# Kernel optimization log

Hardware: AMD Instinct MI355X
Metric: run time of the kernel (lower is better)

Reference implementation:

```python
import jax, jax.numpy as jnp
import numpy as np

PATCH = 8
EPS = 1e-5


def setup_inputs() -> dict:
    key = jax.random.key(0)
    k0, k1, k2 = jax.random.split(key, 3)
    B, C, H, W = 8, 256, 256, 256
    r = 8
    x = jax.random.normal(k0, (B, C, H, W), dtype=jnp.float32)
    gamma = jnp.ones((C,), dtype=jnp.float32)   # LayerNorm weight
    beta = jnp.zeros((C,), dtype=jnp.float32)   # LayerNorm bias
    # torch Linear weights: [out, in], bias=False
    w1 = jax.random.normal(k1, (C // r, C), dtype=jnp.float32) * (1.0 / np.sqrt(C))
    w2 = jax.random.normal(k2, (C, C // r), dtype=jnp.float32) * (1.0 / np.sqrt(C // r))
    return {"x": x, "gamma": gamma, "beta": beta, "w1": w1, "w2": w2}


def reference(x, gamma, beta, w1, w2):
    # x: [B, C, H, W]; H, W divisible by PATCH (no-pad path of the module)
    B, C, H, W = x.shape
    ph = pw = PATCH
    nH, nW = H // ph, W // pw

    # LayerNorm over channel dim (module permutes patches to channel-last before norm;
    # per-pixel channel LN is invariant to the patch regrouping)
    xcl = jnp.transpose(x, (0, 2, 3, 1))                    # [B, H, W, C]
    mu = jnp.mean(xcl, axis=-1, keepdims=True)
    var = jnp.mean(jnp.square(xcl - mu), axis=-1, keepdims=True)
    xn = (xcl - mu) * jax.lax.rsqrt(var + EPS) * gamma + beta

    # patchify: [B, nH, ph, nW, pw, C]
    xp = xn.reshape(B, nH, ph, nW, pw, C)

    # per-patch, per-channel mean of the normalized tensor -> [B, nH, nW, C]
    pm = jnp.mean(xp, axis=(2, 4))

    # SE-style gating MLP (Linear no bias -> SiLU -> Linear no bias -> sigmoid)
    h = jax.nn.silu(jnp.einsum('bijc,rc->bijr', pm, w1))    # [B, nH, nW, C//r]
    gate = jax.nn.sigmoid(jnp.einsum('bijr,cr->bijc', h, w2))  # [B, nH, nW, C]

    # scale normalized patches by per-patch channel gates and scatter back
    out = xp * gate[:, :, None, :, None, :]                 # [B, nH, ph, nW, pw, C]
    out = out.reshape(B, H, W, C)
    return jnp.transpose(out, (0, 3, 1, 2))                 # [B, C, H, W]
```

## Files before the change

kernel.cpp:

```cpp
#include <hip/hip_runtime.h>
#include <hip/hip_bf16.h>
#include <math.h>

#define C_DIM 256
#define HWDIM 256
#define CH_STRIDE (HWDIM * HWDIM)
#define R_DIM 32

typedef float nfloat4 __attribute__((ext_vector_type(4)));

__global__ __launch_bounds__(1024, 4)
void lpa_fused_kernel(const float* __restrict__ x,
                      const float* __restrict__ gamma,
                      const float* __restrict__ beta,
                      const float* __restrict__ w1,
                      const float* __restrict__ w2,
                      float* __restrict__ out)
{
    __shared__ float sp[16 * 256];
    __shared__ float sq[16 * 256];
    __shared__ float mu_s[256];
    __shared__ float rs_s[256];
    __shared__ float gs[C_DIM];
    __shared__ float bs[C_DIM];
    __shared__ float pm_s[4 * C_DIM];
    __shared__ float h_s[4 * R_DIM];
    __shared__ float2 AB_s[4 * C_DIM];

    const int t    = threadIdx.x;
    const int wid  = t >> 6;
    const int lane = t & 63;
    const int hh   = lane >> 3;
    const int wq   = lane & 7;
    const int pat  = wq >> 1;
    const int p0   = hh * 32 + wq * 4;

    const int bid = blockIdx.x;
    const int b   = bid >> 8;
    const int ij  = bid & 255;
    const unsigned H0 = (unsigned)(ij >> 3) * 8u;
    const unsigned W0 = (unsigned)(ij & 7) * 32u;
    const unsigned baseb  = (unsigned)b * (C_DIM * CH_STRIDE);
    const unsigned rowoff = baseb + (H0 + hh) * HWDIM + W0 + (unsigned)wq * 4u;

    if (t < C_DIM) { gs[t] = gamma[t]; bs[t] = beta[t]; }

    const float* xb = x + rowoff + (unsigned)wid * 16u * CH_STRIDE;

    __hip_bfloat162 vlo[16], vhi[16];
    float s0 = 0.f, s1 = 0.f, s2 = 0.f, s3 = 0.f;
    float q0 = 0.f, q1 = 0.f, q2 = 0.f, q3 = 0.f;
#pragma unroll
    for (int k = 0; k < 16; ++k) {
        float4 f = *reinterpret_cast<const float4*>(xb + (unsigned)k * CH_STRIDE);
        s0 += f.x; q0 += f.x * f.x;
        s1 += f.y; q1 += f.y * f.y;
        s2 += f.z; q2 += f.z * f.z;
        s3 += f.w; q3 += f.w * f.w;
        vlo[k] = __float22bfloat162_rn(make_float2(f.x, f.y));
        vhi[k] = __float22bfloat162_rn(make_float2(f.z, f.w));
    }
    *reinterpret_cast<float4*>(&sp[wid * 256 + p0]) = make_float4(s0, s1, s2, s3);
    *reinterpret_cast<float4*>(&sq[wid * 256 + p0]) = make_float4(q0, q1, q2, q3);
    __syncthreads();

    if (t < 256) {
        float s = 0.f, q = 0.f;
#pragma unroll
        for (int w = 0; w < 16; ++w) {
            s += sp[w * 256 + t];
            q += sq[w * 256 + t];
        }
        float mu  = s * (1.0f / 256.0f);
        float var = q * (1.0f / 256.0f) - mu * mu;
        mu_s[t] = mu;
        rs_s[t] = rsqrtf(var + 1e-5f);
    }
    __syncthreads();

    {
        const float4 mu4 = *reinterpret_cast<const float4*>(&mu_s[p0]);
        const float4 rs4 = *reinterpret_cast<const float4*>(&rs_s[p0]);
#pragma unroll
        for (int k = 0; k < 16; ++k) {
            int c = wid * 16 + k;
            float2 xy = __bfloat1622float2(vlo[k]);
            float2 zw = __bfloat1622float2(vhi[k]);
            float wsum = rs4.x * (xy.x - mu4.x) + rs4.y * (xy.y - mu4.y)
                       + rs4.z * (zw.x - mu4.z) + rs4.w * (zw.y - mu4.w);
            wsum += __shfl_xor(wsum, 1);
            wsum += __shfl_xor(wsum, 8);
            wsum += __shfl_xor(wsum, 16);
            wsum += __shfl_xor(wsum, 32);
            if ((lane & 57) == 0) {
                pm_s[pat * C_DIM + c] = gs[c] * wsum * (1.0f / 64.0f) + bs[c];
            }
        }
    }
    __syncthreads();

    {
        const int pat4 = t >> 8;
        const int r    = (t >> 3) & 31;
        const int k8   = t & 7;
        const float4* wrow = reinterpret_cast<const float4*>(w1 + r * C_DIM + k8 * 32);
        const float* pmk = &pm_s[pat4 * C_DIM + k8 * 32];
        float s = 0.f;
#pragma unroll
        for (int j = 0; j < 8; ++j) {
            float4 wv = wrow[j];
            float4 pv = *reinterpret_cast<const float4*>(pmk + j * 4);
            s += wv.x * pv.x + wv.y * pv.y + wv.z * pv.z + wv.w * pv.w;
        }
        s += __shfl_down(s, 4, 8);
        s += __shfl_down(s, 2, 8);
        s += __shfl_down(s, 1, 8);
        if (k8 == 0) {
            float sig = 1.0f / (1.0f + __expf(-s));
            h_s[pat4 * R_DIM + r] = s * sig;
        }
    }
    __syncthreads();

    {
        const int pat4 = t >> 8;
        const int c4   = t & 255;
        const float4* wrow = reinterpret_cast<const float4*>(w2 + c4 * R_DIM);
        const float* hk = &h_s[pat4 * R_DIM];
        float s = 0.f;
#pragma unroll
        for (int j = 0; j < 8; ++j) {
            float4 wv = wrow[j];
            s += wv.x * hk[j * 4 + 0] + wv.y * hk[j * 4 + 1]
               + wv.z * hk[j * 4 + 2] + wv.w * hk[j * 4 + 3];
        }
        float gate = 1.0f / (1.0f + __expf(-s));
        AB_s[pat4 * C_DIM + c4] = make_float2(gs[c4] * gate, bs[c4] * gate);
    }
    __syncthreads();

    {
        const float4 mu4 = *reinterpret_cast<const float4*>(&mu_s[p0]);
        const float4 rs4 = *reinterpret_cast<const float4*>(&rs_s[p0]);
        float* ob = out + rowoff + (unsigned)wid * 16u * CH_STRIDE;
#pragma unroll
        for (int k = 0; k < 16; ++k) {
            int c = wid * 16 + k;
            float2 ab = AB_s[pat * C_DIM + c];
            float2 xy = __bfloat1622float2(vlo[k]);
            float2 zw = __bfloat1622float2(vhi[k]);
            nfloat4 o;
            o.x = ab.x * rs4.x * (xy.x - mu4.x) + ab.y;
            o.y = ab.x * rs4.y * (xy.y - mu4.y) + ab.y;
            o.z = ab.x * rs4.z * (zw.x - mu4.z) + ab.y;
            o.w = ab.x * rs4.w * (zw.y - mu4.w) + ab.y;
            __builtin_nontemporal_store(o,
                reinterpret_cast<nfloat4*>(ob + (unsigned)k * CH_STRIDE));
        }
    }
}

extern "C" void kernel_launch(void* const* d_in, const int* in_sizes, int n_in,
                              void* d_out, int out_size, void* d_ws, size_t ws_size,
                              hipStream_t stream) {
    const float* x     = (const float*)d_in[0];
    const float* gamma = (const float*)d_in[1];
    const float* beta  = (const float*)d_in[2];
    const float* w1    = (const float*)d_in[3];
    const float* w2    = (const float*)d_in[4];
    float* out = (float*)d_out;

    const int B = in_sizes[0] / (C_DIM * HWDIM * HWDIM);
    const int nwg = B * 256;

    lpa_fused_kernel<<<nwg, 1024, 0, stream>>>(x, gamma, beta, w1, w2, out);
}
```

Before: 253.1 us.

## Make blocks persistent over eight tiles and prefetch next tile during gating

Each block now loops over eight 8x32 spatial tiles along a row strip instead of handling one tile, with the grid hard-coded to 256 blocks. The float4 loads for the next tile are issued into registers before the gating MLP of the current tile, so memory latency can overlap the serial reduction/MLP phases. Launch bounds drop to 2 waves-per-EU, allowing more registers for the extra prefetch buffer at the cost of lower occupancy. The fixed grid of 256 assumes batch 8.

```diff
diff --git a/kernel.cpp b/kernel.cpp
--- a/kernel.cpp
+++ b/kernel.cpp
@@ -9,7 +9,7 @@
 
 typedef float nfloat4 __attribute__((ext_vector_type(4)));
 
-__global__ __launch_bounds__(1024, 4)
+__global__ __launch_bounds__(1024, 2)
 void lpa_fused_kernel(const float* __restrict__ x,
                       const float* __restrict__ gamma,
                       const float* __restrict__ beta,
@@ -35,128 +35,155 @@
     const int pat  = wq >> 1;
     const int p0   = hh * 32 + wq * 4;
 
-    const int bid = blockIdx.x;
-    const int b   = bid >> 8;
-    const int ij  = bid & 255;
-    const unsigned H0 = (unsigned)(ij >> 3) * 8u;
-    const unsigned W0 = (unsigned)(ij & 7) * 32u;
-    const unsigned baseb  = (unsigned)b * (C_DIM * CH_STRIDE);
-    const unsigned rowoff = baseb + (H0 + hh) * HWDIM + W0 + (unsigned)wq * 4u;
+    const int bid  = blockIdx.x;
+    const int bimg = bid >> 5;
+    const int H0c  = (bid & 31) * 8;
+    const unsigned ubase = (unsigned)bimg * (C_DIM * CH_STRIDE)
+                         + (unsigned)(H0c + hh) * HWDIM
+                         + (unsigned)wq * 4u
+                         + (unsigned)wid * 16u * CH_STRIDE;
+    const float* xb0 = x + ubase;
+    float* ob0 = out + ubase;
 
     if (t < C_DIM) { gs[t] = gamma[t]; bs[t] = beta[t]; }
 
-    const float* xb = x + rowoff + (unsigned)wid * 16u * CH_STRIDE;
-
+    float4 nv[16];
+#pragma unroll
+    for (int k = 0; k < 16; ++k)
+        nv[k] = *reinterpret_cast<const float4*>(xb0 + (unsigned)k * CH_STRIDE);
     __hip_bfloat162 vlo[16], vhi[16];
-    float s0 = 0.f, s1 = 0.f, s2 = 0.f, s3 = 0.f;
-    float q0 = 0.f, q1 = 0.f, q2 = 0.f, q3 = 0.f;
-#pragma unroll
-    for (int k = 0; k < 16; ++k) {
-        float4 f = *reinterpret_cast<const float4*>(xb + (unsigned)k * CH_STRIDE);
-        s0 += f.x; q0 += f.x * f.x;
-        s1 += f.y; q1 += f.y * f.y;
-        s2 += f.z; q2 += f.z * f.z;
-        s3 += f.w; q3 += f.w * f.w;
-        vlo[k] = __float22bfloat162_rn(make_float2(f.x, f.y));
-        vhi[k] = __float22bfloat162_rn(make_float2(f.z, f.w));
-    }
-    *reinterpret_cast<float4*>(&sp[wid * 256 + p0]) = make_float4(s0, s1, s2, s3);
-    *reinterpret_cast<float4*>(&sq[wid * 256 + p0]) = make_float4(q0, q1, q2, q3);
-    __syncthreads();
-
-    if (t < 256) {
-        float s = 0.f, q = 0.f;
-#pragma unroll
-        for (int w = 0; w < 16; ++w) {
-            s += sp[w * 256 + t];
-            q += sq[w * 256 + t];
-        }
-        float mu  = s * (1.0f / 256.0f);
-        float var = q * (1.0f / 256.0f) - mu * mu;
-        mu_s[t] = mu;
-        rs_s[t] = rsqrtf(var + 1e-5f);
+    {
+        float s0 = 0.f, s1 = 0.f, s2 = 0.f, s3 = 0.f;
+        float q0 = 0.f, q1 = 0.f, q2 = 0.f, q3 = 0.f;
+#pragma unroll
+        for (int k = 0; k < 16; ++k) {
+            float4 f = nv[k];
+            s0 += f.x; q0 += f.x * f.x;
+            s1 += f.y; q1 += f.y * f.y;
+            s2 += f.z; q2 += f.z * f.z;
+            s3 += f.w; q3 += f.w * f.w;
+            vlo[k] = __float22bfloat162_rn(make_float2(f.x, f.y));
+            vhi[k] = __float22bfloat162_rn(make_float2(f.z, f.w));
+        }
+        *reinterpret_cast<float4*>(&sp[wid * 256 + p0]) = make_float4(s0, s1, s2, s3);
+        *reinterpret_cast<float4*>(&sq[wid * 256 + p0]) = make_float4(q0, q1, q2, q3);
     }
     __syncthreads();
 
-    {
+    for (int g = 0; g < 8; ++g) {
+        if (t < 256) {
+            float s = 0.f, q = 0.f;
+#pragma unroll
+            for (int w = 0; w < 16; ++w) {
+                s += sp[w * 256 + t];
+                q += sq[w * 256 + t];
+            }
+            float mu  = s * (1.0f / 256.0f);
+            float var = q * (1.0f / 256.0f) - mu * mu;
+            mu_s[t] = mu;
+            rs_s[t] = rsqrtf(var + 1e-5f);
+        }
+        if (g < 7) {
+            const float* xn = xb0 + (unsigned)(g + 1) * 32u;
+#pragma unroll
+            for (int k = 0; k < 16; ++k)
+                nv[k] = *reinterpret_cast<const float4*>(xn + (unsigned)k * CH_STRIDE);
+        }
+        __syncthreads();
+
         const float4 mu4 = *reinterpret_cast<const float4*>(&mu_s[p0]);
         const float4 rs4 = *reinterpret_cast<const float4*>(&rs_s[p0]);
+
 #pragma unroll
         for (int k = 0; k < 16; ++k) {
             int c = wid * 16 + k;
             float2 xy = __bfloat1622float2(vlo[k]);
             float2 zw = __bfloat1622float2(vhi[k]);
-            float wsum = rs4.x * (xy.x - mu4.x) + rs4.y * (xy.y - mu4.y)
-                       + rs4.z * (zw.x - mu4.z) + rs4.w * (zw.y - mu4.w);
-            wsum += __shfl_xor(wsum, 1);
-            wsum += __shfl_xor(wsum, 8);
-            wsum += __shfl_xor(wsum, 16);
-            wsum += __shfl_xor(wsum, 32);
-            if ((lane & 57) == 0) {
-                pm_s[pat * C_DIM + c] = gs[c] * wsum * (1.0f / 64.0f) + bs[c];
-            }
-        }
-    }
-    __syncthreads();
-
-    {
-        const int pat4 = t >> 8;
-        const int r    = (t >> 3) & 31;
-        const int k8   = t & 7;
-        const float4* wrow = reinterpret_cast<const float4*>(w1 + r * C_DIM + k8 * 32);
-        const float* pmk = &pm_s[pat4 * C_DIM + k8 * 32];
-        float s = 0.f;
-#pragma unroll
-        for (int j = 0; j < 8; ++j) {
-            float4 wv = wrow[j];
-            float4 pv = *reinterpret_cast<const float4*>(pmk + j * 4);
-            s += wv.x * pv.x + wv.y * pv.y + wv.z * pv.z + wv.w * pv.w;
-        }
-        s += __shfl_down(s, 4, 8);
-        s += __shfl_down(s, 2, 8);
-        s += __shfl_down(s, 1, 8);
-        if (k8 == 0) {
-            float sig = 1.0f / (1.0f + __expf(-s));
-            h_s[pat4 * R_DIM + r] = s * sig;
-        }
-    }
-    __syncthreads();
-
-    {
-        const int pat4 = t >> 8;
-        const int c4   = t & 255;
-        const float4* wrow = reinterpret_cast<const float4*>(w2 + c4 * R_DIM);
-        const float* hk = &h_s[pat4 * R_DIM];
-        float s = 0.f;
-#pragma unroll
-        for (int j = 0; j < 8; ++j) {
-            float4 wv = wrow[j];
-            s += wv.x * hk[j * 4 + 0] + wv.y * hk[j * 4 + 1]
-               + wv.z * hk[j * 4 + 2] + wv.w * hk[j * 4 + 3];
-        }
-        float gate = 1.0f / (1.0f + __expf(-s));
-        AB_s[pat4 * C_DIM + c4] = make_float2(gs[c4] * gate, bs[c4] * gate);
-    }
-    __syncthreads();
-
-    {
-        const float4 mu4 = *reinterpret_cast<const float4*>(&mu_s[p0]);
-        const float4 rs4 = *reinterpret_cast<const float4*>(&rs_s[p0]);
-        float* ob = out + rowoff + (unsigned)wid * 16u * CH_STRIDE;
-#pragma unroll
-        for (int k = 0; k < 16; ++k) {
-            int c = wid * 16 + k;
-            float2 ab = AB_s[pat * C_DIM + c];
-            float2 xy = __bfloat1622float2(vlo[k]);
-            float2 zw = __bfloat1622float2(vhi[k]);
-            nfloat4 o;
-            o.x = ab.x * rs4.x * (xy.x - mu4.x) + ab.y;
-            o.y = ab.x * rs4.y * (xy.y - mu4.y) + ab.y;
-            o.z = ab.x * rs4.z * (zw.x - mu4.z) + ab.y;
-            o.w = ab.x * rs4.w * (zw.y - mu4.w) + ab.y;
-            __builtin_nontemporal_store(o,
-                reinterpret_cast<nfloat4*>(ob + (unsigned)k * CH_STRIDE));
-        }
+            float ws = rs4.x * (xy.x - mu4.x) + rs4.y * (xy.y - mu4.y)
+                     + rs4.z * (zw.x - mu4.z) + rs4.w * (zw.y - mu4.w);
+            ws += __shfl_xor(ws, 1);
+            ws += __shfl_xor(ws, 8);
+            ws += __shfl_xor(ws, 16);
+            ws += __shfl_xor(ws, 32);
+            if ((lane & 57) == 0)
+                pm_s[pat * C_DIM + c] = gs[c] * ws * (1.0f / 64.0f) + bs[c];
+        }
+        __syncthreads();
+
+        {
+            const int pat4 = t >> 8;
+            const int r    = (t >> 3) & 31;
+            const int k8   = t & 7;
+            const float4* wrow = reinterpret_cast<const float4*>(w1 + r * C_DIM + k8 * 32);
+            const float* pmk = &pm_s[pat4 * C_DIM + k8 * 32];
+            float s = 0.f;
+#pragma unroll
+            for (int j = 0; j < 8; ++j) {
+                float4 wv = wrow[j];
+                float4 pv = *reinterpret_cast<const float4*>(pmk + j * 4);
+                s += wv.x * pv.x + wv.y * pv.y + wv.z * pv.z + wv.w * pv.w;
+            }
+            s += __shfl_down(s, 4, 8);
+            s += __shfl_down(s, 2, 8);
+            s += __shfl_down(s, 1, 8);
+            if (k8 == 0) {
+                float sig = 1.0f / (1.0f + __expf(-s));
+                h_s[pat4 * R_DIM + r] = s * sig;
+            }
+        }
+        __syncthreads();
+
+        {
+            const int pat4 = t >> 8;
+            const int c4   = t & 255;
+            const float4* wrow = reinterpret_cast<const float4*>(w2 + c4 * R_DIM);
+            const float* hk = &h_s[pat4 * R_DIM];
+            float s = 0.f;
+#pragma unroll
+            for (int j = 0; j < 8; ++j) {
+                float4 wv = wrow[j];
+                s += wv.x * hk[j * 4 + 0] + wv.y * hk[j * 4 + 1]
+                   + wv.z * hk[j * 4 + 2] + wv.w * hk[j * 4 + 3];
+            }
+            float gate = 1.0f / (1.0f + __expf(-s));
+            AB_s[pat4 * C_DIM + c4] = make_float2(gs[c4] * gate, bs[c4] * gate);
+        }
+        __syncthreads();
+
+        {
+            float* ob = ob0 + (unsigned)g * 32u;
+#pragma unroll
+            for (int k = 0; k < 16; ++k) {
+                int c = wid * 16 + k;
+                float2 ab = AB_s[pat * C_DIM + c];
+                float2 xy = __bfloat1622float2(vlo[k]);
+                float2 zw = __bfloat1622float2(vhi[k]);
+                nfloat4 o;
+                o.x = ab.x * rs4.x * (xy.x - mu4.x) + ab.y;
+                o.y = ab.x * rs4.y * (xy.y - mu4.y) + ab.y;
+                o.z = ab.x * rs4.z * (zw.x - mu4.z) + ab.y;
+                o.w = ab.x * rs4.w * (zw.y - mu4.w) + ab.y;
+                __builtin_nontemporal_store(o,
+                    reinterpret_cast<nfloat4*>(ob + (unsigned)k * CH_STRIDE));
+            }
+        }
+        if (g < 7) {
+            float s0 = 0.f, s1 = 0.f, s2 = 0.f, s3 = 0.f;
+            float q0 = 0.f, q1 = 0.f, q2 = 0.f, q3 = 0.f;
+#pragma unroll
+            for (int k = 0; k < 16; ++k) {
+                float4 f = nv[k];
+                s0 += f.x; q0 += f.x * f.x;
+                s1 += f.y; q1 += f.y * f.y;
+                s2 += f.z; q2 += f.z * f.z;
+                s3 += f.w; q3 += f.w * f.w;
+                vlo[k] = __float22bfloat162_rn(make_float2(f.x, f.y));
+                vhi[k] = __float22bfloat162_rn(make_float2(f.z, f.w));
+            }
+            *reinterpret_cast<float4*>(&sp[wid * 256 + p0]) = make_float4(s0, s1, s2, s3);
+            *reinterpret_cast<float4*>(&sq[wid * 256 + p0]) = make_float4(q0, q1, q2, q3);
+        }
+        __syncthreads();
     }
 }
 
@@ -170,8 +197,5 @@
     const float* w2    = (const float*)d_in[4];
     float* out = (float*)d_out;
 
-    const int B = in_sizes[0] / (C_DIM * HWDIM * HWDIM);
-    const int nwg = B * 256;
-
-    lpa_fused_kernel<<<nwg, 1024, 0, stream>>>(x, gamma, beta, w1, w2, out);
+    lpa_fused_kernel<<<256, 1024, 0, stream>>>(x, gamma, beta, w1, w2, out);
 }
```

Result: slower. 687.6 us (+171.6%).

## Stage bf16 tile in LDS instead of registers; atomic LDS stats reduction

Applied to the files above, without the earlier changes.

Each thread now stores its bf16-rounded values in a padded shared-memory tile rather than holding 32 packed registers. The per-pixel sum and sum-of-squares partials are combined with LDS atomics instead of a 16-way shared reduction. The per-patch channel mean is computed by one thread per (channel, patch) reading the LDS tile, replacing the wavefront shuffle reductions. The goal is lower register pressure and fewer shuffles, but the tile takes about 130KB of LDS, which limits each CU to one 1024-thread block and reduces occupancy. The launch_bounds hint is also dropped.

```diff
diff --git a/kernel.cpp b/kernel.cpp
--- a/kernel.cpp
+++ b/kernel.cpp
@@ -6,10 +6,11 @@
 #define HWDIM 256
 #define CH_STRIDE (HWDIM * HWDIM)
 #define R_DIM 32
+#define PXW 130
 
 typedef float nfloat4 __attribute__((ext_vector_type(4)));
 
-__global__ __launch_bounds__(1024, 4)
+__global__
 void lpa_fused_kernel(const float* __restrict__ x,
                       const float* __restrict__ gamma,
                       const float* __restrict__ beta,
@@ -17,8 +18,9 @@
                       const float* __restrict__ w2,
                       float* __restrict__ out)
 {
-    __shared__ float sp[16 * 256];
-    __shared__ float sq[16 * 256];
+    __shared__ __hip_bfloat162 xl[C_DIM * PXW];
+    __shared__ float sp1[256];
+    __shared__ float sq1[256];
     __shared__ float mu_s[256];
     __shared__ float rs_s[256];
     __shared__ float gs[C_DIM];
@@ -34,20 +36,20 @@
     const int wq   = lane & 7;
     const int pat  = wq >> 1;
     const int p0   = hh * 32 + wq * 4;
+    const int p2   = p0 >> 1;
+
+    if (t < 256) { sp1[t] = 0.f; sq1[t] = 0.f; gs[t] = gamma[t]; bs[t] = beta[t]; }
+    __syncthreads();
 
     const int bid = blockIdx.x;
     const int b   = bid >> 8;
     const int ij  = bid & 255;
     const unsigned H0 = (unsigned)(ij >> 3) * 8u;
     const unsigned W0 = (unsigned)(ij & 7) * 32u;
-    const unsigned baseb  = (unsigned)b * (C_DIM * CH_STRIDE);
-    const unsigned rowoff = baseb + (H0 + hh) * HWDIM + W0 + (unsigned)wq * 4u;
-
-    if (t < C_DIM) { gs[t] = gamma[t]; bs[t] = beta[t]; }
-
+    const unsigned rowoff = (unsigned)b * (C_DIM * CH_STRIDE)
+                          + (H0 + (unsigned)hh) * HWDIM + W0 + (unsigned)wq * 4u;
     const float* xb = x + rowoff + (unsigned)wid * 16u * CH_STRIDE;
 
-    __hip_bfloat162 vlo[16], vhi[16];
     float s0 = 0.f, s1 = 0.f, s2 = 0.f, s3 = 0.f;
     float q0 = 0.f, q1 = 0.f, q2 = 0.f, q3 = 0.f;
 #pragma unroll
@@ -57,45 +59,46 @@
         s1 += f.y; q1 += f.y * f.y;
         s2 += f.z; q2 += f.z * f.z;
         s3 += f.w; q3 += f.w * f.w;
-        vlo[k] = __float22bfloat162_rn(make_float2(f.x, f.y));
-        vhi[k] = __float22bfloat162_rn(make_float2(f.z, f.w));
+        __hip_bfloat162 lo = __float22bfloat162_rn(make_float2(f.x, f.y));
+        __hip_bfloat162 hi = __float22bfloat162_rn(make_float2(f.z, f.w));
+        uint2 wv;
+        wv.x = *reinterpret_cast<const unsigned*>(&lo);
+        wv.y = *reinterpret_cast<const unsigned*>(&hi);
+        const int c = wid * 16 + k;
+        *reinterpret_cast<uint2*>(&xl[c * PXW + p2]) = wv;
     }
-    *reinterpret_cast<float4*>(&sp[wid * 256 + p0]) = make_float4(s0, s1, s2, s3);
-    *reinterpret_cast<float4*>(&sq[wid * 256 + p0]) = make_float4(q0, q1, q2, q3);
+    atomicAdd(&sp1[p0 + 0], s0); atomicAdd(&sq1[p0 + 0], q0);
+    atomicAdd(&sp1[p0 + 1], s1); atomicAdd(&sq1[p0 + 1], q1);
+    atomicAdd(&sp1[p0 + 2], s2); atomicAdd(&sq1[p0 + 2], q2);
+    atomicAdd(&sp1[p0 + 3], s3); atomicAdd(&sq1[p0 + 3], q3);
     __syncthreads();
 
     if (t < 256) {
-        float s = 0.f, q = 0.f;
-#pragma unroll
-        for (int w = 0; w < 16; ++w) {
-            s += sp[w * 256 + t];
-            q += sq[w * 256 + t];
-        }
-        float mu  = s * (1.0f / 256.0f);
-        float var = q * (1.0f / 256.0f) - mu * mu;
+        float mu  = sp1[t] * (1.0f / 256.0f);
+        float var = sq1[t] * (1.0f / 256.0f) - mu * mu;
         mu_s[t] = mu;
         rs_s[t] = rsqrtf(var + 1e-5f);
     }
     __syncthreads();
 
     {
-        const float4 mu4 = *reinterpret_cast<const float4*>(&mu_s[p0]);
-        const float4 rs4 = *reinterpret_cast<const float4*>(&rs_s[p0]);
+        const int c  = t & 255;
+        const int pt = t >> 8;
+        const __hip_bfloat162* row = &xl[c * PXW];
+        float acc = 0.f;
 #pragma unroll
-        for (int k = 0; k < 16; ++k) {
-            int c = wid * 16 + k;
-            float2 xy = __bfloat1622float2(vlo[k]);
-            float2 zw = __bfloat1622float2(vhi[k]);
-            float wsum = rs4.x * (xy.x - mu4.x) + rs4.y * (xy.y - mu4.y)
-                       + rs4.z * (zw.x - mu4.z) + rs4.w * (zw.y - mu4.w);
-            wsum += __shfl_xor(wsum, 1);
-            wsum += __shfl_xor(wsum, 8);
-            wsum += __shfl_xor(wsum, 16);
-            wsum += __shfl_xor(wsum, 32);
-            if ((lane & 57) == 0) {
-                pm_s[pat * C_DIM + c] = gs[c] * wsum * (1.0f / 64.0f) + bs[c];
+        for (int h2 = 0; h2 < 8; ++h2) {
+            const int pbase = h2 * 32 + pt * 8;
+            const int wbase = (pbase >> 1);
+#pragma unroll
+            for (int j = 0; j < 4; ++j) {
+                float2 xy = __bfloat1622float2(row[wbase + j]);
+                const int p = pbase + j * 2;
+                acc += rs_s[p]     * (xy.x - mu_s[p])
+                     + rs_s[p + 1] * (xy.y - mu_s[p + 1]);
             }
         }
+        pm_s[pt * C_DIM + c] = gs[c] * acc * (1.0f / 64.0f) + bs[c];
     }
     __syncthreads();
 
@@ -145,10 +148,13 @@
         float* ob = out + rowoff + (unsigned)wid * 16u * CH_STRIDE;
 #pragma unroll
         for (int k = 0; k < 16; ++k) {
-            int c = wid * 16 + k;
+            const int c = wid * 16 + k;
             float2 ab = AB_s[pat * C_DIM + c];
-            float2 xy = __bfloat1622float2(vlo[k]);
-            float2 zw = __bfloat1622float2(vhi[k]);
+            uint2 wv = *reinterpret_cast<const uint2*>(&xl[c * PXW + p2]);
+            __hip_bfloat162 lo = *reinterpret_cast<const __hip_bfloat162*>(&wv.x);
+            __hip_bfloat162 hi = *reinterpret_cast<const __hip_bfloat162*>(&wv.y);
+            float2 xy = __bfloat1622float2(lo);
+            float2 zw = __bfloat1622float2(hi);
             nfloat4 o;
             o.x = ab.x * rs4.x * (xy.x - mu4.x) + ab.y;
             o.y = ab.x * rs4.y * (xy.y - mu4.y) + ab.y;
```

Result: slower. 272.5 us (+7.7%).
